# Kernel tuning notes

Hardware: AMD Instinct MI355X
Metric: run time of the kernel (lower is better)

Reference implementation:

```python
import jax, jax.numpy as jnp
import numpy as np

EPS = 1e-06


def setup_inputs() -> dict:
    key = jax.random.key(0)
    ks = jax.random.split(key, 8)
    B, T, D = 4, 1024, 1024  # module requires T == D (diagonal einsum)
    s = 1.0 / np.sqrt(D)
    return {
        "x_seq": jax.random.normal(ks[0], (B, T, D), dtype=jnp.float32),
        "gamma": jnp.asarray(0.9, dtype=jnp.float32),
        "Wq": jax.random.normal(ks[1], (D, D), dtype=jnp.float32) * s,
        "bq": jax.random.normal(ks[2], (D,), dtype=jnp.float32) * 0.01,
        "Wk": jax.random.normal(ks[3], (D, D), dtype=jnp.float32) * s,
        "bk": jax.random.normal(ks[4], (D,), dtype=jnp.float32) * 0.01,
        "Wv": jax.random.normal(ks[5], (D, D), dtype=jnp.float32) * s,
        "bv": jax.random.normal(ks[6], (D,), dtype=jnp.float32) * 0.01,
    }


def reference(x_seq, gamma, Wq, bq, Wk, bk, Wv, bv):
    # Faithful math of SUPRAParallelFixedGamma.forward. Notes on fidelity:
    # - torch einsum 'ij,bjdj->bidj' takes the DIAGONAL of kv over (time, last
    #   v-dim), i.e. kv[b,j,d,j] = k[b,j,d] * v[b,j,j]; requires T == D.
    # - gamma_exponents = arange(T)[None,:] - arange(T)[:,None] -> E[i,j] = max(j-i, 0)
    #   (the clamp leaves PAST entries at gamma**0 == 1 and decays FUTURE ones).
    # - S = cumsum over dim 1 (the 'i'/time-output axis) then contracted with q;
    #   this factors exactly as C = cumsum(G, axis=0) applied as a (T,T) weight,
    #   avoiding the original's O(B*T*D*T) intermediate while computing the same math.
    B, T, D = x_seq.shape
    q = jax.nn.relu(x_seq @ Wq.T + bq)          # phi(W_q x)
    k = jax.nn.relu(x_seq @ Wk.T + bk)          # phi(W_k x)
    v = x_seq @ Wv.T + bv
    t = jnp.arange(T)
    E = jnp.maximum(t[None, :] - t[:, None], 0).astype(x_seq.dtype)  # (T,T)
    G = gamma ** E                               # gamma_powers[i,j] = gamma**max(j-i,0)
    C = jnp.cumsum(G, axis=0)                    # C[t,j] = sum_{t'<=t} G[t',j]
    vd = jnp.diagonal(v, axis1=1, axis2=2)       # (B,T): v[b,j,j]  (T==D)
    kv_diag = k * vd[:, :, None]                 # (B,T,D): kv[b,j,d,j]
    # num[b,t,j] = sum_d q[b,t,d] * C[t,j] * kv_diag[b,j,d]
    num = C[None, :, :] * jnp.einsum('btd,bjd->btj', q, kv_diag)
    # Z[b,t,d] = cumsum_t of (G @ k) = sum_j C[t,j] k[b,j,d]
    Z = jnp.einsum('tj,bjd->btd', C, k)
    denom = jnp.sum(q * Z, axis=-1, keepdims=True) + EPS
    return num / denom
```

## Files before the change

### kernel.cpp

```cpp
#include <hip/hip_runtime.h>

typedef __attribute__((ext_vector_type(8))) short bf16x8;
typedef __attribute__((ext_vector_type(4))) float f32x4;


__device__ __forceinline__ unsigned short f2bf(float f) {
    unsigned int u = __builtin_bit_cast(unsigned int, f);
    u += 0x7fffu + ((u >> 16) & 1u);
    return (unsigned short)(u >> 16);
}

__device__ __forceinline__ float bf2f(unsigned short s) {
    return __builtin_bit_cast(float, (unsigned int)s << 16);
}

__device__ __forceinline__ void g2lds16(const unsigned short* g, unsigned short* l) {
    __builtin_amdgcn_global_load_lds(
        (const __attribute__((address_space(1))) unsigned int*)g,
        (__attribute__((address_space(3))) unsigned int*)l, 16, 0, 0);
}


__global__ __launch_bounds__(256)
void pack3_kernel(const float* __restrict__ x, const float* __restrict__ wq,
                  const float* __restrict__ wk, unsigned short* __restrict__ xb,
                  unsigned short* __restrict__ wqk, int n4x, int n4w) {
    int i = blockIdx.x * 256 + threadIdx.x;
    const float* src; unsigned short* dst; int idx;
    if (i < n4x)            { src = x;  dst = xb;  idx = i; }
    else if (i < n4x + n4w) { src = wq; dst = wqk; idx = i - n4x; }
    else                    { src = wk; dst = wqk + (size_t)n4w * 4; idx = i - n4x - n4w; }
    float4 v = reinterpret_cast<const float4*>(src)[idx];
    union { unsigned short s[4]; uint2 u; } o;
    o.s[0] = f2bf(v.x); o.s[1] = f2bf(v.y); o.s[2] = f2bf(v.z); o.s[3] = f2bf(v.w);
    reinterpret_cast<uint2*>(dst)[idx] = o.u;
}


__global__ __launch_bounds__(256)
void vdiag_kernel(const unsigned short* __restrict__ xb, const float* __restrict__ Wv,
                  const float* __restrict__ bv, float* __restrict__ vd) {
    int w = blockIdx.x * 4 + (threadIdx.x >> 6);
    int lane = threadIdx.x & 63;
    int b = w >> 10, j = w & 1023;
    const unsigned short* xr = xb + (size_t)(b * 1024 + j) * 1024;
    const float* wr = Wv + (size_t)j * 1024;
    float s = 0.f;
    #pragma unroll
    for (int e = 0; e < 2; ++e) {
        int base = e * 512 + lane * 8;
        bf16x8 xv = *reinterpret_cast<const bf16x8*>(xr + base);
        float4 w0 = *reinterpret_cast<const float4*>(wr + base);
        float4 w1 = *reinterpret_cast<const float4*>(wr + base + 4);
        s = fmaf(bf2f((unsigned short)xv[0]), w0.x, s);
        s = fmaf(bf2f((unsigned short)xv[1]), w0.y, s);
        s = fmaf(bf2f((unsigned short)xv[2]), w0.z, s);
        s = fmaf(bf2f((unsigned short)xv[3]), w0.w, s);
        s = fmaf(bf2f((unsigned short)xv[4]), w1.x, s);
        s = fmaf(bf2f((unsigned short)xv[5]), w1.y, s);
        s = fmaf(bf2f((unsigned short)xv[6]), w1.z, s);
        s = fmaf(bf2f((unsigned short)xv[7]), w1.w, s);
    }
    #pragma unroll
    for (int off = 32; off; off >>= 1) s += __shfl_down(s, off, 64);
    if (lane == 0) vd[w] = s + bv[j];
}


__global__ __launch_bounds__(256, 4)
void gemm_qk_kernel(const unsigned short* __restrict__ A, const unsigned short* __restrict__ Bm,
                    unsigned short* __restrict__ qb, unsigned short* __restrict__ kb,
                    const float* __restrict__ bq, const float* __restrict__ bk, int K) {
    __shared__ unsigned short lA[2][128 * 32];
    __shared__ unsigned short lB[2][64 * 32];

    const int tid = threadIdx.x;
    const int lane = tid & 63;
    const int wid = tid >> 6;
    const int wr = wid >> 1;
    const int wc = wid & 1;
    const int tileM = blockIdx.y * 128, tileN = blockIdx.x * 64;

    const int r0 = tid >> 2;
    const int r1 = (tid + 256) >> 2;
    const int cc = (tid & 3) * 8;
    const int frow = lane & 15;
    const int fk = (lane >> 4) * 8;

    f32x4 acc[4][2];
    #pragma unroll
    for (int m = 0; m < 4; ++m)
        #pragma unroll
        for (int n = 0; n < 2; ++n)
            acc[m][n] = (f32x4){0.f, 0.f, 0.f, 0.f};

    auto stage = [&](int buf, int k0) {
        g2lds16(A + (size_t)(tileM + r0) * K + (k0 + cc), &lA[buf][tid * 8]);
        g2lds16(A + (size_t)(tileM + r1) * K + (k0 + cc), &lA[buf][2048 + tid * 8]);
        g2lds16(Bm + (size_t)(tileN + r0) * K + (k0 + cc), &lB[buf][tid * 8]);
    };

    stage(0, 0);
    __syncthreads();
    int cur = 0;
    for (int k0 = 0; k0 < K; k0 += 32) {
        if (k0 + 32 < K) stage(cur ^ 1, k0 + 32);

        bf16x8 af[4], bfr[2];
        #pragma unroll
        for (int m = 0; m < 4; ++m)
            af[m] = *reinterpret_cast<const bf16x8*>(&lA[cur][(wr * 64 + m * 16 + frow) * 32 + fk]);
        #pragma unroll
        for (int n = 0; n < 2; ++n)
            bfr[n] = *reinterpret_cast<const bf16x8*>(&lB[cur][(wc * 32 + n * 16 + frow) * 32 + fk]);

        #pragma unroll
        for (int m = 0; m < 4; ++m)
            #pragma unroll
            for (int n = 0; n < 2; ++n)
                acc[m][n] = __builtin_amdgcn_mfma_f32_16x16x32_bf16(af[m], bfr[n], acc[m][n], 0, 0, 0);

        __syncthreads();
        cur ^= 1;
    }

    const int orow = (lane >> 4) * 4;
    const int ocol = lane & 15;
    const bool isQ = tileN < 1024;
    unsigned short* Cq = isQ ? qb : kb;
    const float* bias = isQ ? bq : bk;
    const int cb = tileN - (isQ ? 0 : 1024);

    #pragma unroll
    for (int n = 0; n < 2; ++n) {
        int col = cb + wc * 32 + n * 16 + ocol;
        float bia = bias[col];
        #pragma unroll
        for (int m = 0; m < 4; ++m) {
            #pragma unroll
            for (int i = 0; i < 4; ++i) {
                int row = tileM + wr * 64 + m * 16 + orow + i;
                float v = acc[m][n][i] + bia;
                Cq[(size_t)row * 1024 + col] = f2bf(v > 0.f ? v : 0.f);
            }
        }
    }
}


__global__ __launch_bounds__(256, 2)
void gemm_attn_kernel(const unsigned short* __restrict__ A, const unsigned short* __restrict__ Bm,
                      unsigned short* __restrict__ nmb, const float* __restrict__ vd,
                      float* __restrict__ dpart, const float* __restrict__ gammap,
                      int K, int Mtot) {
    __shared__ unsigned short lA[2][64 * 32];
    __shared__ unsigned short lB[2][128 * 32];

    const int tid = threadIdx.x;
    const int lane = tid & 63;
    const int wid = tid >> 6;
    const int wr = wid >> 1, wc = wid & 1;
    const int tileM = blockIdx.y * 64, tileN = blockIdx.x * 128;

    const unsigned short* Ab = A + (size_t)blockIdx.z * 1024 * 1024;
    const unsigned short* Bb = Bm + (size_t)blockIdx.z * 1024 * 1024;

    const int r0 = tid >> 2;
    const int r1 = (tid + 256) >> 2;
    const int cc = (tid & 3) * 8;
    const int frow = lane & 15;
    const int fk = (lane >> 4) * 8;

    f32x4 acc[2][4];
    #pragma unroll
    for (int m = 0; m < 2; ++m)
        #pragma unroll
        for (int n = 0; n < 4; ++n)
            acc[m][n] = (f32x4){0.f, 0.f, 0.f, 0.f};

    auto stage = [&](int buf, int k0) {
        g2lds16(Ab + (size_t)(tileM + r0) * K + (k0 + cc), &lA[buf][tid * 8]);
        g2lds16(Bb + (size_t)(tileN + r0) * K + (k0 + cc), &lB[buf][tid * 8]);
        g2lds16(Bb + (size_t)(tileN + r1) * K + (k0 + cc), &lB[buf][2048 + tid * 8]);
    };

    stage(0, 0);
    __syncthreads();
    int cur = 0;
    for (int k0 = 0; k0 < K; k0 += 32) {
        if (k0 + 32 < K) stage(cur ^ 1, k0 + 32);

        bf16x8 af[2], bfr[4];
        #pragma unroll
        for (int m = 0; m < 2; ++m)
            af[m] = *reinterpret_cast<const bf16x8*>(&lA[cur][(wr * 32 + m * 16 + frow) * 32 + fk]);
        #pragma unroll
        for (int n = 0; n < 4; ++n)
            bfr[n] = *reinterpret_cast<const bf16x8*>(&lB[cur][(wc * 64 + n * 16 + frow) * 32 + fk]);

        #pragma unroll
        for (int m = 0; m < 2; ++m)
            #pragma unroll
            for (int n = 0; n < 4; ++n)
                acc[m][n] = __builtin_amdgcn_mfma_f32_16x16x32_bf16(af[m], bfr[n], acc[m][n], 0, 0, 0);

        __syncthreads();
        cur ^= 1;
    }

    const int orow = (lane >> 4) * 4;
    const int ocol = lane & 15;

    unsigned short* ob = nmb + (size_t)blockIdx.z * 1024 * 1024;
    const float* vdb = vd + blockIdx.z * 1024;
    const float g = gammap[0];
    const float l2g = log2f(g);
    const float inv1mg = 1.f / (1.f - g);
    const float c1 = g * inv1mg;

    int jcol[4]; float gj[4], vdv[4];
    #pragma unroll
    for (int n = 0; n < 4; ++n) {
        jcol[n] = tileN + wc * 64 + n * 16 + ocol;
        gj[n] = exp2f((float)jcol[n] * l2g);
        vdv[n] = vdb[jcol[n]];
    }

    #pragma unroll
    for (int m = 0; m < 2; ++m) {
        #pragma unroll
        for (int i = 0; i < 4; ++i) {
            int t = tileM + wr * 32 + m * 16 + orow + i;
            float gt = exp2f((float)t * l2g);
            float ctf = (1.f - g * gt) * inv1mg;
            float s = 0.f;
            #pragma unroll
            for (int n = 0; n < 4; ++n) {
                int j = jcol[n];
                float Cfut = exp2f((float)(j - t) * l2g) * ctf;
                float Cpast = (float)(t - j + 1) + c1 * (1.f - gj[n]);
                float Cw = (j <= t) ? Cpast : Cfut;
                float v = acc[m][n][i];
                s += Cw * v;
                ob[(size_t)t * 1024 + j] = f2bf(Cw * vdv[n] * v);
            }
            s += __shfl_xor(s, 1, 64);
            s += __shfl_xor(s, 2, 64);
            s += __shfl_xor(s, 4, 64);
            s += __shfl_xor(s, 8, 64);
            if ((lane & 15) == 0)
                dpart[(size_t)(blockIdx.x * 2 + wc) * Mtot + blockIdx.z * 1024 + t] = s;
        }
    }
}


__global__ __launch_bounds__(256)
void scale_kernel(const unsigned short* __restrict__ nmb, float* __restrict__ out,
                  const float* __restrict__ dpart, int Mtot) {
    int r = blockIdx.x;
    float s = 1e-6f;
    #pragma unroll
    for (int p = 0; p < 16; ++p) s += dpart[(size_t)p * Mtot + r];
    float inv = 1.f / s;
    const uint2* src = reinterpret_cast<const uint2*>(nmb + (size_t)r * 1024);
    float4* dst = reinterpret_cast<float4*>(out + (size_t)r * 1024);
    uint2 u = src[threadIdx.x];
    float4 v = { bf2f((unsigned short)(u.x & 0xffff)) * inv,
                 bf2f((unsigned short)(u.x >> 16))    * inv,
                 bf2f((unsigned short)(u.y & 0xffff)) * inv,
                 bf2f((unsigned short)(u.y >> 16))    * inv };
    dst[threadIdx.x] = v;
}


extern "C" void kernel_launch(void* const* d_in, const int* in_sizes, int n_in,
                              void* d_out, int out_size, void* d_ws, size_t ws_size,
                              hipStream_t stream) {
    const float* x     = (const float*)d_in[0];
    const float* gamma = (const float*)d_in[1];
    const float* Wq    = (const float*)d_in[2];
    const float* bq    = (const float*)d_in[3];
    const float* Wk    = (const float*)d_in[4];
    const float* bk    = (const float*)d_in[5];
    const float* Wv    = (const float*)d_in[6];
    const float* bv    = (const float*)d_in[7];
    float* out = (float*)d_out;

    const int D = 1024, T = 1024;
    const int B = in_sizes[0] / (T * D);
    const int M = B * T;

    char* ws = (char*)d_ws;
    size_t off = 0;
    unsigned short* xb  = (unsigned short*)(ws + off); off += (size_t)M * D * 2;
    unsigned short* wqk = (unsigned short*)(ws + off); off += (size_t)2 * D * D * 2;
    unsigned short* qb  = (unsigned short*)(ws + off); off += (size_t)M * D * 2;
    unsigned short* kb  = (unsigned short*)(ws + off); off += (size_t)M * D * 2;
    float* vd    = (float*)(ws + off); off += (size_t)M * 4;
    float* dpart = (float*)(ws + off); off += (size_t)16 * M * 4;
    unsigned short* nmb = xb;

    const int n4x = M * D / 4, n4w = D * D / 4;

    pack3_kernel<<<dim3((n4x + 2 * n4w) / 256), 256, 0, stream>>>(x, Wq, Wk, xb, wqk, n4x, n4w);

    vdiag_kernel<<<dim3(M / 4), 256, 0, stream>>>(xb, Wv, bv, vd);

    gemm_qk_kernel<<<dim3(2048 / 64, M / 128), 256, 0, stream>>>(
        xb, wqk, qb, kb, bq, bk, D);

    gemm_attn_kernel<<<dim3(T / 128, T / 64, B), 256, 0, stream>>>(
        qb, kb, nmb, vd, dpart, gamma, D, M);

    scale_kernel<<<dim3(M), 256, 0, stream>>>(nmb, out, dpart, M);
}
```

Baseline: 76.23 us.

## Fuse pack and v-diagonal kernels; double GEMM K-tile to 64

Merges the bf16 pack kernel and the v-diagonal dot-product kernel into one launch. The diagonal part now reads fp32 x directly, so it no longer depends on the packed copy. Both MFMA GEMMs move from a K-step of 32 to 64, which halves the number of barriers and loop iterations but doubles LDS per block. The occupancy hint for the qk GEMM drops from 4 to 3 and for the attention GEMM rises from 2 to 3. The larger LDS footprint may limit how many blocks fit per CU, and the 128-byte LDS rows may cause bank conflicts.

```diff
diff --git a/kernel.cpp b/kernel.cpp
--- a/kernel.cpp
+++ b/kernel.cpp
@@ -22,57 +22,46 @@
 
 
 __global__ __launch_bounds__(256)
-void pack3_kernel(const float* __restrict__ x, const float* __restrict__ wq,
-                  const float* __restrict__ wk, unsigned short* __restrict__ xb,
-                  unsigned short* __restrict__ wqk, int n4x, int n4w) {
-    int i = blockIdx.x * 256 + threadIdx.x;
-    const float* src; unsigned short* dst; int idx;
-    if (i < n4x)            { src = x;  dst = xb;  idx = i; }
-    else if (i < n4x + n4w) { src = wq; dst = wqk; idx = i - n4x; }
-    else                    { src = wk; dst = wqk + (size_t)n4w * 4; idx = i - n4x - n4w; }
-    float4 v = reinterpret_cast<const float4*>(src)[idx];
-    union { unsigned short s[4]; uint2 u; } o;
-    o.s[0] = f2bf(v.x); o.s[1] = f2bf(v.y); o.s[2] = f2bf(v.z); o.s[3] = f2bf(v.w);
-    reinterpret_cast<uint2*>(dst)[idx] = o.u;
-}
-
-
-__global__ __launch_bounds__(256)
-void vdiag_kernel(const unsigned short* __restrict__ xb, const float* __restrict__ Wv,
-                  const float* __restrict__ bv, float* __restrict__ vd) {
-    int w = blockIdx.x * 4 + (threadIdx.x >> 6);
-    int lane = threadIdx.x & 63;
-    int b = w >> 10, j = w & 1023;
-    const unsigned short* xr = xb + (size_t)(b * 1024 + j) * 1024;
-    const float* wr = Wv + (size_t)j * 1024;
-    float s = 0.f;
-    #pragma unroll
-    for (int e = 0; e < 2; ++e) {
-        int base = e * 512 + lane * 8;
-        bf16x8 xv = *reinterpret_cast<const bf16x8*>(xr + base);
-        float4 w0 = *reinterpret_cast<const float4*>(wr + base);
-        float4 w1 = *reinterpret_cast<const float4*>(wr + base + 4);
-        s = fmaf(bf2f((unsigned short)xv[0]), w0.x, s);
-        s = fmaf(bf2f((unsigned short)xv[1]), w0.y, s);
-        s = fmaf(bf2f((unsigned short)xv[2]), w0.z, s);
-        s = fmaf(bf2f((unsigned short)xv[3]), w0.w, s);
-        s = fmaf(bf2f((unsigned short)xv[4]), w1.x, s);
-        s = fmaf(bf2f((unsigned short)xv[5]), w1.y, s);
-        s = fmaf(bf2f((unsigned short)xv[6]), w1.z, s);
-        s = fmaf(bf2f((unsigned short)xv[7]), w1.w, s);
-    }
-    #pragma unroll
-    for (int off = 32; off; off >>= 1) s += __shfl_down(s, off, 64);
-    if (lane == 0) vd[w] = s + bv[j];
-}
-
-
-__global__ __launch_bounds__(256, 4)
+void prep_kernel(const float* __restrict__ x, const float* __restrict__ wq,
+                 const float* __restrict__ wk, const float* __restrict__ Wv,
+                 const float* __restrict__ bv, unsigned short* __restrict__ xb,
+                 unsigned short* __restrict__ wqk, float* __restrict__ vd,
+                 int n4x, int n4w, int npack) {
+    if ((int)blockIdx.x < npack) {
+        int i = blockIdx.x * 256 + threadIdx.x;
+        const float* src; unsigned short* dst; int idx;
+        if (i < n4x)            { src = x;  dst = xb;  idx = i; }
+        else if (i < n4x + n4w) { src = wq; dst = wqk; idx = i - n4x; }
+        else                    { src = wk; dst = wqk + (size_t)n4w * 4; idx = i - n4x - n4w; }
+        float4 v = reinterpret_cast<const float4*>(src)[idx];
+        union { unsigned short s[4]; uint2 u; } o;
+        o.s[0] = f2bf(v.x); o.s[1] = f2bf(v.y); o.s[2] = f2bf(v.z); o.s[3] = f2bf(v.w);
+        reinterpret_cast<uint2*>(dst)[idx] = o.u;
+    } else {
+        int w = (blockIdx.x - npack) * 4 + (threadIdx.x >> 6);
+        int lane = threadIdx.x & 63;
+        int b = w >> 10, j = w & 1023;
+        const float4* xr = reinterpret_cast<const float4*>(x + (size_t)(b * 1024 + j) * 1024);
+        const float4* wr = reinterpret_cast<const float4*>(Wv + (size_t)j * 1024);
+        float s = 0.f;
+        #pragma unroll
+        for (int e = 0; e < 4; ++e) {
+            float4 a = xr[lane + 64 * e], c = wr[lane + 64 * e];
+            s += a.x * c.x + a.y * c.y + a.z * c.z + a.w * c.w;
+        }
+        #pragma unroll
+        for (int off = 32; off; off >>= 1) s += __shfl_down(s, off, 64);
+        if (lane == 0) vd[w] = s + bv[j];
+    }
+}
+
+
+__global__ __launch_bounds__(256, 3)
 void gemm_qk_kernel(const unsigned short* __restrict__ A, const unsigned short* __restrict__ Bm,
                     unsigned short* __restrict__ qb, unsigned short* __restrict__ kb,
                     const float* __restrict__ bq, const float* __restrict__ bk, int K) {
-    __shared__ unsigned short lA[2][128 * 32];
-    __shared__ unsigned short lB[2][64 * 32];
+    __shared__ unsigned short lA[2][128 * 64];
+    __shared__ unsigned short lB[2][64 * 64];
 
     const int tid = threadIdx.x;
     const int lane = tid & 63;
@@ -81,9 +70,8 @@
     const int wc = wid & 1;
     const int tileM = blockIdx.y * 128, tileN = blockIdx.x * 64;
 
-    const int r0 = tid >> 2;
-    const int r1 = (tid + 256) >> 2;
-    const int cc = (tid & 3) * 8;
+    const int srow = tid >> 3;
+    const int scol = (tid & 7) * 8;
     const int frow = lane & 15;
     const int fk = (lane >> 4) * 8;
 
@@ -95,30 +83,43 @@
             acc[m][n] = (f32x4){0.f, 0.f, 0.f, 0.f};
 
     auto stage = [&](int buf, int k0) {
-        g2lds16(A + (size_t)(tileM + r0) * K + (k0 + cc), &lA[buf][tid * 8]);
-        g2lds16(A + (size_t)(tileM + r1) * K + (k0 + cc), &lA[buf][2048 + tid * 8]);
-        g2lds16(Bm + (size_t)(tileN + r0) * K + (k0 + cc), &lB[buf][tid * 8]);
+        #pragma unroll
+        for (int j = 0; j < 4; ++j)
+            g2lds16(A + (size_t)(tileM + j * 32 + srow) * K + (k0 + scol),
+                    &lA[buf][(j * 32 + srow) * 64 + scol]);
+        #pragma unroll
+        for (int j = 0; j < 2; ++j)
+            g2lds16(Bm + (size_t)(tileN + j * 32 + srow) * K + (k0 + scol),
+                    &lB[buf][(j * 32 + srow) * 64 + scol]);
     };
 
     stage(0, 0);
     __syncthreads();
     int cur = 0;
-    for (int k0 = 0; k0 < K; k0 += 32) {
-        if (k0 + 32 < K) stage(cur ^ 1, k0 + 32);
-
-        bf16x8 af[4], bfr[2];
-        #pragma unroll
-        for (int m = 0; m < 4; ++m)
-            af[m] = *reinterpret_cast<const bf16x8*>(&lA[cur][(wr * 64 + m * 16 + frow) * 32 + fk]);
-        #pragma unroll
-        for (int n = 0; n < 2; ++n)
-            bfr[n] = *reinterpret_cast<const bf16x8*>(&lB[cur][(wc * 32 + n * 16 + frow) * 32 + fk]);
-
-        #pragma unroll
-        for (int m = 0; m < 4; ++m)
+    for (int k0 = 0; k0 < K; k0 += 64) {
+        if (k0 + 64 < K) stage(cur ^ 1, k0 + 64);
+
+        bf16x8 af[2][4], bfr[2][2];
+        #pragma unroll
+        for (int kk = 0; kk < 2; ++kk) {
+            #pragma unroll
+            for (int m = 0; m < 4; ++m)
+                af[kk][m] = *reinterpret_cast<const bf16x8*>(
+                    &lA[cur][(wr * 64 + m * 16 + frow) * 64 + kk * 32 + fk]);
             #pragma unroll
             for (int n = 0; n < 2; ++n)
-                acc[m][n] = __builtin_amdgcn_mfma_f32_16x16x32_bf16(af[m], bfr[n], acc[m][n], 0, 0, 0);
+                bfr[kk][n] = *reinterpret_cast<const bf16x8*>(
+                    &lB[cur][(wc * 32 + n * 16 + frow) * 64 + kk * 32 + fk]);
+        }
+
+        #pragma unroll
+        for (int kk = 0; kk < 2; ++kk)
+            #pragma unroll
+            for (int m = 0; m < 4; ++m)
+                #pragma unroll
+                for (int n = 0; n < 2; ++n)
+                    acc[m][n] = __builtin_amdgcn_mfma_f32_16x16x32_bf16(
+                        af[kk][m], bfr[kk][n], acc[m][n], 0, 0, 0);
 
         __syncthreads();
         cur ^= 1;
@@ -148,13 +149,13 @@
 }
 
 
-__global__ __launch_bounds__(256, 2)
+__global__ __launch_bounds__(256, 3)
 void gemm_attn_kernel(const unsigned short* __restrict__ A, const unsigned short* __restrict__ Bm,
                       unsigned short* __restrict__ nmb, const float* __restrict__ vd,
                       float* __restrict__ dpart, const float* __restrict__ gammap,
                       int K, int Mtot) {
-    __shared__ unsigned short lA[2][64 * 32];
-    __shared__ unsigned short lB[2][128 * 32];
+    __shared__ unsigned short lA[2][64 * 64];
+    __shared__ unsigned short lB[2][128 * 64];
 
     const int tid = threadIdx.x;
     const int lane = tid & 63;
@@ -165,9 +166,8 @@
     const unsigned short* Ab = A + (size_t)blockIdx.z * 1024 * 1024;
     const unsigned short* Bb = Bm + (size_t)blockIdx.z * 1024 * 1024;
 
-    const int r0 = tid >> 2;
-    const int r1 = (tid + 256) >> 2;
-    const int cc = (tid & 3) * 8;
+    const int srow = tid >> 3;
+    const int scol = (tid & 7) * 8;
     const int frow = lane & 15;
     const int fk = (lane >> 4) * 8;
 
@@ -179,30 +179,43 @@
             acc[m][n] = (f32x4){0.f, 0.f, 0.f, 0.f};
 
     auto stage = [&](int buf, int k0) {
-        g2lds16(Ab + (size_t)(tileM + r0) * K + (k0 + cc), &lA[buf][tid * 8]);
-        g2lds16(Bb + (size_t)(tileN + r0) * K + (k0 + cc), &lB[buf][tid * 8]);
-        g2lds16(Bb + (size_t)(tileN + r1) * K + (k0 + cc), &lB[buf][2048 + tid * 8]);
+        #pragma unroll
+        for (int j = 0; j < 2; ++j)
+            g2lds16(Ab + (size_t)(tileM + j * 32 + srow) * K + (k0 + scol),
+                    &lA[buf][(j * 32 + srow) * 64 + scol]);
+        #pragma unroll
+        for (int j = 0; j < 4; ++j)
+            g2lds16(Bb + (size_t)(tileN + j * 32 + srow) * K + (k0 + scol),
+                    &lB[buf][(j * 32 + srow) * 64 + scol]);
     };
 
     stage(0, 0);
     __syncthreads();
     int cur = 0;
-    for (int k0 = 0; k0 < K; k0 += 32) {
-        if (k0 + 32 < K) stage(cur ^ 1, k0 + 32);
-
-        bf16x8 af[2], bfr[4];
-        #pragma unroll
-        for (int m = 0; m < 2; ++m)
-            af[m] = *reinterpret_cast<const bf16x8*>(&lA[cur][(wr * 32 + m * 16 + frow) * 32 + fk]);
-        #pragma unroll
-        for (int n = 0; n < 4; ++n)
-            bfr[n] = *reinterpret_cast<const bf16x8*>(&lB[cur][(wc * 64 + n * 16 + frow) * 32 + fk]);
-
-        #pragma unroll
-        for (int m = 0; m < 2; ++m)
+    for (int k0 = 0; k0 < K; k0 += 64) {
+        if (k0 + 64 < K) stage(cur ^ 1, k0 + 64);
+
+        bf16x8 af[2][2], bfr[2][4];
+        #pragma unroll
+        for (int kk = 0; kk < 2; ++kk) {
+            #pragma unroll
+            for (int m = 0; m < 2; ++m)
+                af[kk][m] = *reinterpret_cast<const bf16x8*>(
+                    &lA[cur][(wr * 32 + m * 16 + frow) * 64 + kk * 32 + fk]);
             #pragma unroll
             for (int n = 0; n < 4; ++n)
-                acc[m][n] = __builtin_amdgcn_mfma_f32_16x16x32_bf16(af[m], bfr[n], acc[m][n], 0, 0, 0);
+                bfr[kk][n] = *reinterpret_cast<const bf16x8*>(
+                    &lB[cur][(wc * 64 + n * 16 + frow) * 64 + kk * 32 + fk]);
+        }
+
+        #pragma unroll
+        for (int kk = 0; kk < 2; ++kk)
+            #pragma unroll
+            for (int m = 0; m < 2; ++m)
+                #pragma unroll
+                for (int n = 0; n < 4; ++n)
+                    acc[m][n] = __builtin_amdgcn_mfma_f32_16x16x32_bf16(
+                        af[kk][m], bfr[kk][n], acc[m][n], 0, 0, 0);
 
         __syncthreads();
         cur ^= 1;
@@ -302,10 +315,10 @@
     unsigned short* nmb = xb;
 
     const int n4x = M * D / 4, n4w = D * D / 4;
-
-    pack3_kernel<<<dim3((n4x + 2 * n4w) / 256), 256, 0, stream>>>(x, Wq, Wk, xb, wqk, n4x, n4w);
-
-    vdiag_kernel<<<dim3(M / 4), 256, 0, stream>>>(xb, Wv, bv, vd);
+    const int npack = (n4x + 2 * n4w) / 256;
+
+    prep_kernel<<<dim3(npack + M / 4), 256, 0, stream>>>(
+        x, Wq, Wk, Wv, bv, xb, wqk, vd, n4x, n4w, npack);
 
     gemm_qk_kernel<<<dim3(2048 / 64, M / 128), 256, 0, stream>>>(
         xb, wqk, qb, kb, bq, bk, D);
```

After: 86.19 us. 13.1% more time.

## Fuse pack and vdiag kernels, enlarge QK GEMM tile with swizzled LDS

Applied to the files above, without the earlier changes.

Merges the bf16 packing kernel and the v-diagonal kernel into one launch, with vdiag now reading fp32 x directly instead of the packed bf16 copy. The QK projection GEMM tile grows from 128x64 to 128x128 so each block reuses its loads across more output columns. LDS reads and writes use an XOR swizzle on the k-chunk to avoid bank conflicts. Occupancy hints change as well: the QK GEMM drops to 2 blocks per CU and the attention GEMM rises to 3, trading register budget for occupancy.

```diff
diff --git a/kernel.cpp b/kernel.cpp
--- a/kernel.cpp
+++ b/kernel.cpp
@@ -22,82 +22,73 @@
 
 
 __global__ __launch_bounds__(256)
-void pack3_kernel(const float* __restrict__ x, const float* __restrict__ wq,
-                  const float* __restrict__ wk, unsigned short* __restrict__ xb,
-                  unsigned short* __restrict__ wqk, int n4x, int n4w) {
-    int i = blockIdx.x * 256 + threadIdx.x;
-    const float* src; unsigned short* dst; int idx;
-    if (i < n4x)            { src = x;  dst = xb;  idx = i; }
-    else if (i < n4x + n4w) { src = wq; dst = wqk; idx = i - n4x; }
-    else                    { src = wk; dst = wqk + (size_t)n4w * 4; idx = i - n4x - n4w; }
-    float4 v = reinterpret_cast<const float4*>(src)[idx];
-    union { unsigned short s[4]; uint2 u; } o;
-    o.s[0] = f2bf(v.x); o.s[1] = f2bf(v.y); o.s[2] = f2bf(v.z); o.s[3] = f2bf(v.w);
-    reinterpret_cast<uint2*>(dst)[idx] = o.u;
-}
-
-
-__global__ __launch_bounds__(256)
-void vdiag_kernel(const unsigned short* __restrict__ xb, const float* __restrict__ Wv,
-                  const float* __restrict__ bv, float* __restrict__ vd) {
-    int w = blockIdx.x * 4 + (threadIdx.x >> 6);
-    int lane = threadIdx.x & 63;
-    int b = w >> 10, j = w & 1023;
-    const unsigned short* xr = xb + (size_t)(b * 1024 + j) * 1024;
-    const float* wr = Wv + (size_t)j * 1024;
-    float s = 0.f;
-    #pragma unroll
-    for (int e = 0; e < 2; ++e) {
-        int base = e * 512 + lane * 8;
-        bf16x8 xv = *reinterpret_cast<const bf16x8*>(xr + base);
-        float4 w0 = *reinterpret_cast<const float4*>(wr + base);
-        float4 w1 = *reinterpret_cast<const float4*>(wr + base + 4);
-        s = fmaf(bf2f((unsigned short)xv[0]), w0.x, s);
-        s = fmaf(bf2f((unsigned short)xv[1]), w0.y, s);
-        s = fmaf(bf2f((unsigned short)xv[2]), w0.z, s);
-        s = fmaf(bf2f((unsigned short)xv[3]), w0.w, s);
-        s = fmaf(bf2f((unsigned short)xv[4]), w1.x, s);
-        s = fmaf(bf2f((unsigned short)xv[5]), w1.y, s);
-        s = fmaf(bf2f((unsigned short)xv[6]), w1.z, s);
-        s = fmaf(bf2f((unsigned short)xv[7]), w1.w, s);
-    }
-    #pragma unroll
-    for (int off = 32; off; off >>= 1) s += __shfl_down(s, off, 64);
-    if (lane == 0) vd[w] = s + bv[j];
-}
-
-
-__global__ __launch_bounds__(256, 4)
+void prep_kernel(const float* __restrict__ x, const float* __restrict__ wq,
+                 const float* __restrict__ wk, const float* __restrict__ Wv,
+                 const float* __restrict__ bv, unsigned short* __restrict__ xb,
+                 unsigned short* __restrict__ wqk, float* __restrict__ vd,
+                 int n4x, int n4w, int npack) {
+    if ((int)blockIdx.x < npack) {
+        int i = blockIdx.x * 256 + threadIdx.x;
+        const float* src; unsigned short* dst; int idx;
+        if (i < n4x)            { src = x;  dst = xb;  idx = i; }
+        else if (i < n4x + n4w) { src = wq; dst = wqk; idx = i - n4x; }
+        else                    { src = wk; dst = wqk + (size_t)n4w * 4; idx = i - n4x - n4w; }
+        float4 v = reinterpret_cast<const float4*>(src)[idx];
+        union { unsigned short s[4]; uint2 u; } o;
+        o.s[0] = f2bf(v.x); o.s[1] = f2bf(v.y); o.s[2] = f2bf(v.z); o.s[3] = f2bf(v.w);
+        reinterpret_cast<uint2*>(dst)[idx] = o.u;
+    } else {
+        int w = (blockIdx.x - npack) * 4 + (threadIdx.x >> 6);
+        int lane = threadIdx.x & 63;
+        int b = w >> 10, j = w & 1023;
+        const float4* xr = reinterpret_cast<const float4*>(x + (size_t)(b * 1024 + j) * 1024);
+        const float4* wr = reinterpret_cast<const float4*>(Wv + (size_t)j * 1024);
+        float s = 0.f;
+        #pragma unroll
+        for (int e = 0; e < 4; ++e) {
+            float4 a = xr[lane + 64 * e], c = wr[lane + 64 * e];
+            s += a.x * c.x + a.y * c.y + a.z * c.z + a.w * c.w;
+        }
+        #pragma unroll
+        for (int off = 32; off; off >>= 1) s += __shfl_down(s, off, 64);
+        if (lane == 0) vd[w] = s + bv[j];
+    }
+}
+
+
+__global__ __launch_bounds__(256, 2)
 void gemm_qk_kernel(const unsigned short* __restrict__ A, const unsigned short* __restrict__ Bm,
                     unsigned short* __restrict__ qb, unsigned short* __restrict__ kb,
                     const float* __restrict__ bq, const float* __restrict__ bk, int K) {
     __shared__ unsigned short lA[2][128 * 32];
-    __shared__ unsigned short lB[2][64 * 32];
+    __shared__ unsigned short lB[2][128 * 32];
 
     const int tid = threadIdx.x;
     const int lane = tid & 63;
     const int wid = tid >> 6;
     const int wr = wid >> 1;
     const int wc = wid & 1;
-    const int tileM = blockIdx.y * 128, tileN = blockIdx.x * 64;
-
-    const int r0 = tid >> 2;
-    const int r1 = (tid + 256) >> 2;
-    const int cc = (tid & 3) * 8;
+    const int tileM = blockIdx.y * 128, tileN = blockIdx.x * 128;
+
+    const int srow = tid >> 2;
+    const int scolL = (tid & 3) * 8;
+    const int scolG = ((tid & 3) ^ (srow & 3)) * 8;
     const int frow = lane & 15;
-    const int fk = (lane >> 4) * 8;
-
-    f32x4 acc[4][2];
+    const int fq = lane >> 4;
+    const int gR = (fq ^ (frow & 3)) * 8;
+
+    f32x4 acc[4][4];
     #pragma unroll
     for (int m = 0; m < 4; ++m)
         #pragma unroll
-        for (int n = 0; n < 2; ++n)
+        for (int n = 0; n < 4; ++n)
             acc[m][n] = (f32x4){0.f, 0.f, 0.f, 0.f};
 
     auto stage = [&](int buf, int k0) {
-        g2lds16(A + (size_t)(tileM + r0) * K + (k0 + cc), &lA[buf][tid * 8]);
-        g2lds16(A + (size_t)(tileM + r1) * K + (k0 + cc), &lA[buf][2048 + tid * 8]);
-        g2lds16(Bm + (size_t)(tileN + r0) * K + (k0 + cc), &lB[buf][tid * 8]);
+        g2lds16(A + (size_t)(tileM + srow) * K + (k0 + scolG),      &lA[buf][srow * 32 + scolL]);
+        g2lds16(A + (size_t)(tileM + 64 + srow) * K + (k0 + scolG), &lA[buf][(64 + srow) * 32 + scolL]);
+        g2lds16(Bm + (size_t)(tileN + srow) * K + (k0 + scolG),     &lB[buf][srow * 32 + scolL]);
+        g2lds16(Bm + (size_t)(tileN + 64 + srow) * K + (k0 + scolG),&lB[buf][(64 + srow) * 32 + scolL]);
     };
 
     stage(0, 0);
@@ -106,18 +97,20 @@
     for (int k0 = 0; k0 < K; k0 += 32) {
         if (k0 + 32 < K) stage(cur ^ 1, k0 + 32);
 
-        bf16x8 af[4], bfr[2];
+        bf16x8 af[4], bfr[4];
         #pragma unroll
         for (int m = 0; m < 4; ++m)
-            af[m] = *reinterpret_cast<const bf16x8*>(&lA[cur][(wr * 64 + m * 16 + frow) * 32 + fk]);
-        #pragma unroll
-        for (int n = 0; n < 2; ++n)
-            bfr[n] = *reinterpret_cast<const bf16x8*>(&lB[cur][(wc * 32 + n * 16 + frow) * 32 + fk]);
+            af[m] = *reinterpret_cast<const bf16x8*>(
+                &lA[cur][(wr * 64 + m * 16 + frow) * 32 + gR]);
+        #pragma unroll
+        for (int n = 0; n < 4; ++n)
+            bfr[n] = *reinterpret_cast<const bf16x8*>(
+                &lB[cur][(wc * 64 + n * 16 + frow) * 32 + gR]);
 
         #pragma unroll
         for (int m = 0; m < 4; ++m)
             #pragma unroll
-            for (int n = 0; n < 2; ++n)
+            for (int n = 0; n < 4; ++n)
                 acc[m][n] = __builtin_amdgcn_mfma_f32_16x16x32_bf16(af[m], bfr[n], acc[m][n], 0, 0, 0);
 
         __syncthreads();
@@ -132,8 +125,8 @@
     const int cb = tileN - (isQ ? 0 : 1024);
 
     #pragma unroll
-    for (int n = 0; n < 2; ++n) {
-        int col = cb + wc * 32 + n * 16 + ocol;
+    for (int n = 0; n < 4; ++n) {
+        int col = cb + wc * 64 + n * 16 + ocol;
         float bia = bias[col];
         #pragma unroll
         for (int m = 0; m < 4; ++m) {
@@ -148,7 +141,7 @@
 }
 
 
-__global__ __launch_bounds__(256, 2)
+__global__ __launch_bounds__(256, 3)
 void gemm_attn_kernel(const unsigned short* __restrict__ A, const unsigned short* __restrict__ Bm,
                       unsigned short* __restrict__ nmb, const float* __restrict__ vd,
                       float* __restrict__ dpart, const float* __restrict__ gammap,
@@ -302,12 +295,12 @@
     unsigned short* nmb = xb;
 
     const int n4x = M * D / 4, n4w = D * D / 4;
-
-    pack3_kernel<<<dim3((n4x + 2 * n4w) / 256), 256, 0, stream>>>(x, Wq, Wk, xb, wqk, n4x, n4w);
-
-    vdiag_kernel<<<dim3(M / 4), 256, 0, stream>>>(xb, Wv, bv, vd);
-
-    gemm_qk_kernel<<<dim3(2048 / 64, M / 128), 256, 0, stream>>>(
+    const int npack = (n4x + 2 * n4w) / 256;
+
+    prep_kernel<<<dim3(npack + M / 4), 256, 0, stream>>>(
+        x, Wq, Wk, Wv, bv, xb, wqk, vd, n4x, n4w, npack);
+
+    gemm_qk_kernel<<<dim3(2048 / 128, M / 128), 256, 0, stream>>>(
         xb, wqk, qb, kb, bq, bk, D);
 
     gemm_attn_kernel<<<dim3(T / 128, T / 64, B), 256, 0, stream>>>(
```

New measurement: 75.13 us. About the same (-1.4%).
